# Kernel tuning notes

Hardware: AMD Instinct MI355X
Metric: run time of the kernel (lower is better)

Reference implementation:

```python
import jax, jax.numpy as jnp
import numpy as np

B, C_IN, L = 8, 64, 4096
C_OUT, HEADS = 64, 3
E = 524288
T_DIM = 256
N = B * L
EPS = 1e-5
NEG_SLOPE = 0.2  # PyG GATConv default negative_slope


def setup_inputs() -> dict:
    key = jax.random.key(0)
    ks = jax.random.split(key, 12)
    x = jax.random.normal(ks[0], (B, C_IN, L), jnp.float32)
    time_emb = jax.random.normal(ks[1], (B, T_DIM), jnp.float32)
    edge_index = jax.random.randint(ks[2], (2, E), 0, N, dtype=jnp.int32)
    # GATConv params: lin maps in -> heads*out; att_src/att_dst per head
    W_lin = jax.random.normal(ks[3], (C_IN, HEADS * C_OUT), jnp.float32) / np.sqrt(C_IN)
    att_src = jax.random.normal(ks[4], (1, HEADS, C_OUT), jnp.float32) / np.sqrt(C_OUT)
    att_dst = jax.random.normal(ks[5], (1, HEADS, C_OUT), jnp.float32) / np.sqrt(C_OUT)
    bias = jnp.zeros((C_OUT,), jnp.float32)
    # time projection (computed but unused in the source forward)
    tp_W = jax.random.normal(ks[6], (T_DIM, C_OUT), jnp.float32) / np.sqrt(T_DIM)
    tp_b = jnp.zeros((C_OUT,), jnp.float32)
    # BatchNorm1d affine params (training-mode batch stats)
    gamma = jnp.ones((C_OUT,), jnp.float32)
    beta = jnp.zeros((C_OUT,), jnp.float32)
    return {"x": x, "time_emb": time_emb, "edge_index": edge_index,
            "W_lin": W_lin, "att_src": att_src, "att_dst": att_dst,
            "bias": bias, "tp_W": tp_W, "tp_b": tp_b,
            "gamma": gamma, "beta": beta}


def reference(x, time_emb, edge_index, W_lin, att_src, att_dst, bias, tp_W, tp_b, gamma, beta):
    b, c, l = x.shape
    n = b * l
    # time projection: present in source but its result is never used
    _t = (time_emb @ tp_W + tp_b)[:, :, None]  # [b, C_OUT, 1] (dead)
    h = (x.reshape(-1, c) @ W_lin).reshape(n, HEADS, C_OUT)  # [N,H,C]
    a_src = (h * att_src).sum(-1)  # [N,H]
    a_dst = (h * att_dst).sum(-1)  # [N,H]
    # add self loops (PyG default add_self_loops=True)
    loops = jnp.arange(n, dtype=edge_index.dtype)
    src = jnp.concatenate([edge_index[0], loops])
    dst = jnp.concatenate([edge_index[1], loops])
    e = a_src[src] + a_dst[dst]                        # [E+N, H]
    e = jnp.where(e > 0, e, NEG_SLOPE * e)             # LeakyReLU
    emax = jax.ops.segment_max(e, dst, num_segments=n)  # every node has a self loop
    ex = jnp.exp(e - emax[dst])
    denom = jax.ops.segment_sum(ex, dst, num_segments=n)
    alpha = ex / denom[dst]                            # segment softmax over dst
    msg = alpha[:, :, None] * h[src]                   # [E+N, H, C]
    out = jax.ops.segment_sum(msg, dst, num_segments=n)  # [N,H,C]
    out = out.mean(axis=1) + bias                      # concat=False -> head mean
    # BatchNorm1d (training mode: biased batch stats)
    mu = out.mean(axis=0)
    var = ((out - mu) ** 2).mean(axis=0)
    out = (out - mu) / jnp.sqrt(var + EPS) * gamma + beta
    out = jax.nn.relu(out)
    return out.reshape(b, -1, l)
```

## Files before the change

kernel.cpp:

```cpp
#include <hip/hip_runtime.h>

#define N_NODES 32768
#define E_EDGES 524288
#define HC 192
#define NEG_SLOPE 0.2f
#define BN_EPS 1e-5f
#define PAD 64

typedef _Float16 f16;
typedef __attribute__((ext_vector_type(8))) _Float16 v8h;
typedef __attribute__((ext_vector_type(4))) float    v4f;

#define SCAT_BLOCKS 512
#define ASCORE_BLOCKS 512
#define FUSED_BLOCKS (SCAT_BLOCKS + ASCORE_BLOCKS)
#define NODE_BLOCKS 8192
#define GEMM_BLOCKS 512
#define APPLY_BLOCKS 512

__device__ __forceinline__ float lrelu(float v) { return v > 0.f ? v : NEG_SLOPE * v; }

__device__ __forceinline__ float wave_sum(float v) {
#pragma unroll
    for (int off = 32; off > 0; off >>= 1) v += __shfl_xor(v, off);
    return v;
}

__global__ __launch_bounds__(256, 4) void k_fused(
        const int* __restrict__ esrc, const int* __restrict__ edst,
        int* __restrict__ cnt, unsigned short* __restrict__ csr_pad,
        const float* __restrict__ x, const float* __restrict__ W,
        const float* __restrict__ att_s, const float* __restrict__ att_d,
        f16* __restrict__ x16, float* __restrict__ a_src, float* __restrict__ a_dst,
        f16* __restrict__ Wp, float* __restrict__ gp1, float* __restrict__ gp2) {
    const int bid = blockIdx.x;
    if (bid < SCAT_BLOCKS) {
        const int base = bid * 1024 + threadIdx.x;
        int s0 = esrc[base];       int d0 = edst[base];
        int s1 = esrc[base + 256]; int d1 = edst[base + 256];
        int s2 = esrc[base + 512]; int d2 = edst[base + 512];
        int s3 = esrc[base + 768]; int d3 = edst[base + 768];
        int p0 = atomicAdd(&cnt[d0], 1);
        int p1 = atomicAdd(&cnt[d1], 1);
        int p2 = atomicAdd(&cnt[d2], 1);
        int p3 = atomicAdd(&cnt[d3], 1);
        if (p0 < PAD) csr_pad[d0 * PAD + p0] = (unsigned short)s0;
        if (p1 < PAD) csr_pad[d1 * PAD + p1] = (unsigned short)s1;
        if (p2 < PAD) csr_pad[d2 * PAD + p2] = (unsigned short)s2;
        if (p3 < PAD) csr_pad[d3 * PAD + p3] = (unsigned short)s3;
        return;
    }
    const int gid = bid - SCAT_BLOCKS;
    __shared__ float us[3][64], ud[3][64];
    if (threadIdx.x < 192) {
        const int h = threadIdx.x >> 6, k = threadIdx.x & 63;
        const float* wr = W + k * HC + h * 64;
        const float* ap = att_s + h * 64;
        const float* dp = att_d + h * 64;
        float su = 0.f, du = 0.f;
#pragma unroll
        for (int ch = 0; ch < 64; ch++) {
            float w = wr[ch];
            su = fmaf(w, ap[ch], su);
            du = fmaf(w, dp[ch], du);
        }
        us[h][k] = su; ud[h][k] = du;
    }
    if (gid == 0) {
        float4 z4 = make_float4(0.f, 0.f, 0.f, 0.f);
#pragma unroll
        for (int i = 0; i < 4; i++) {
            ((float4*)gp1)[threadIdx.x * 4 + i] = z4;
            ((float4*)gp2)[threadIdx.x * 4 + i] = z4;
        }
        for (int idx = threadIdx.x; idx < 1536; idx += 256) {
            const int kfct = idx >> 6, ln = idx & 63;
            const int kf = kfct >> 2, ct = kfct & 3;
            const int qq = ln >> 4, nn = ln & 15;
#pragma unroll
            for (int j = 0; j < 8; j++) {
                int kp = kf * 32 + qq * 8 + j;
                int h = kp >> 6, kk = kp & 63;
                Wp[(size_t)idx * 8 + j] = (f16)W[kk * HC + h * 64 + ct * 16 + nn];
            }
        }
    }
    __syncthreads();
    const int lane = threadIdx.x & 63, wv = threadIdx.x >> 6;
    const float u0 = us[0][lane], u1 = us[1][lane], u2 = us[2][lane];
    const float d0 = ud[0][lane], d1 = ud[1][lane], d2 = ud[2][lane];
    const int nbase = (gid * 4 + wv) * 16;
#pragma unroll 1
    for (int t = 0; t < 16; t++) {
        const int n = nbase + t;
        const float xv = x[n * 64 + lane];
        x16[n * 64 + lane] = (f16)xv;
        float s0 = wave_sum(xv * u0), s1 = wave_sum(xv * u1), s2 = wave_sum(xv * u2);
        float t0 = wave_sum(xv * d0), t1 = wave_sum(xv * d1), t2 = wave_sum(xv * d2);
        if (lane == 0) {
            ((float4*)a_src)[n] = make_float4(s0, s1, s2, 0.f);
            ((float4*)a_dst)[n] = make_float4(t0, t1, t2, 0.f);
        }
    }
}

__global__ __launch_bounds__(256, 8) void k_node(
        const f16* __restrict__ x16,
        const float* __restrict__ a_src,
        const float* __restrict__ a_dst,
        const int* __restrict__ cnt,
        const unsigned short* __restrict__ csr_pad,
        f16* __restrict__ Z) {
    const int lane = threadIdx.x & 63;
    const int wv = threadIdx.x >> 6;
    const int n = blockIdx.x * 4 + wv;

    int deg = cnt[n]; if (deg > PAD) deg = PAD;
    const unsigned short* __restrict__ row = csr_pad + n * PAD;

    const float ad0 = a_dst[n * 4 + 0], ad1 = a_dst[n * 4 + 1], ad2 = a_dst[n * 4 + 2];

    float ws0 = __expf(lrelu(a_src[n * 4 + 0] + ad0));
    float ws1 = __expf(lrelu(a_src[n * 4 + 1] + ad1));
    float ws2 = __expf(lrelu(a_src[n * 4 + 2] + ad2));

    int s = 0;
    float w0 = 0.f, w1 = 0.f, w2 = 0.f;
    if (lane < deg) {
        s = (int)row[lane];
        float4 as = ((const float4*)a_src)[s];
        w0 = __expf(lrelu(as.x + ad0));
        w1 = __expf(lrelu(as.y + ad1));
        w2 = __expf(lrelu(as.z + ad2));
    }
    float den0 = ws0 + wave_sum(w0);
    float den1 = ws1 + wave_sum(w1);
    float den2 = ws2 + wave_sum(w2);
    const float i0 = 1.f / (3.f * den0);
    const float i1 = 1.f / (3.f * den1);
    const float i2 = 1.f / (3.f * den2);

    __shared__ float4 wsl[4][64];
    wsl[wv][lane] = make_float4(w0 * i0, w1 * i1, w2 * i2, __int_as_float(s));

    const float xs = (float)x16[n * 64 + lane];
    float z0 = ws0 * i0 * xs, z1 = ws1 * i1 * xs, z2 = ws2 * i2 * xs;

    int j = 0;
    for (; j + 8 <= deg; j += 8) {
        int sj[8]; float xv[8];
#pragma unroll
        for (int u = 0; u < 8; u++) sj[u] = __builtin_amdgcn_readlane(s, j + u);
#pragma unroll
        for (int u = 0; u < 8; u++) xv[u] = (float)x16[(size_t)sj[u] * 64 + lane];
#pragma unroll
        for (int u = 0; u < 8; u++) {
            float4 wj = wsl[wv][j + u];
            z0 = fmaf(wj.x, xv[u], z0);
            z1 = fmaf(wj.y, xv[u], z1);
            z2 = fmaf(wj.z, xv[u], z2);
        }
    }
    for (; j < deg; j++) {
        int sa = __builtin_amdgcn_readlane(s, j);
        float xa = (float)x16[(size_t)sa * 64 + lane];
        float4 wj = wsl[wv][j];
        z0 = fmaf(wj.x, xa, z0);
        z1 = fmaf(wj.y, xa, z1);
        z2 = fmaf(wj.z, xa, z2);
    }

    f16* zr = Z + (size_t)n * HC;
    zr[lane]       = (f16)z0;
    zr[64 + lane]  = (f16)z1;
    zr[128 + lane] = (f16)z2;
}

__global__ __launch_bounds__(256, 4) void k_gemm(
        const f16* __restrict__ Z, const f16* __restrict__ Wp,
        const float* __restrict__ bias,
        float* __restrict__ out_pre,
        float* __restrict__ gp1, float* __restrict__ gp2) {
    const int lane = threadIdx.x & 63, wv = threadIdx.x >> 6;
    const int q = lane >> 4, nl = lane & 15;
    const int n0 = (blockIdx.x * 4 + wv) * 16;

    v4f C[4] = {{0.f,0.f,0.f,0.f},{0.f,0.f,0.f,0.f},{0.f,0.f,0.f,0.f},{0.f,0.f,0.f,0.f}};
#pragma unroll
    for (int kf = 0; kf < 6; kf++) {
        v8h zb = *(const v8h*)(Z + (size_t)(n0 + nl) * HC + kf * 32 + q * 8);
#pragma unroll
        for (int ct = 0; ct < 4; ct++) {
            v8h wa = *(const v8h*)(Wp + ((size_t)(kf * 4 + ct) * 64 + lane) * 8);
            C[ct] = __builtin_amdgcn_mfma_f32_16x16x32_f16(wa, zb, C[ct], 0, 0, 0);
        }
    }

    __shared__ float bs[4][64], bq[4][64];
#pragma unroll
    for (int ct = 0; ct < 4; ct++) {
        const int ch0 = ct * 16 + q * 4;
        float4 bv = *(const float4*)(bias + ch0);
        float o0 = C[ct][0] + bv.x, o1 = C[ct][1] + bv.y;
        float o2 = C[ct][2] + bv.z, o3 = C[ct][3] + bv.w;
        *(float4*)(out_pre + (size_t)(n0 + nl) * 64 + ch0) = make_float4(o0, o1, o2, o3);
        float r0 = o0, r1 = o1, r2 = o2, r3 = o3;
        float s0 = o0 * o0, s1 = o1 * o1, s2 = o2 * o2, s3 = o3 * o3;
#pragma unroll
        for (int off = 1; off < 16; off <<= 1) {
            r0 += __shfl_xor(r0, off); r1 += __shfl_xor(r1, off);
            r2 += __shfl_xor(r2, off); r3 += __shfl_xor(r3, off);
            s0 += __shfl_xor(s0, off); s1 += __shfl_xor(s1, off);
            s2 += __shfl_xor(s2, off); s3 += __shfl_xor(s3, off);
        }
        if (nl == 0) {
            bs[wv][ch0 + 0] = r0; bs[wv][ch0 + 1] = r1;
            bs[wv][ch0 + 2] = r2; bs[wv][ch0 + 3] = r3;
            bq[wv][ch0 + 0] = s0; bq[wv][ch0 + 1] = s1;
            bq[wv][ch0 + 2] = s2; bq[wv][ch0 + 3] = s3;
        }
    }
    __syncthreads();
    if (threadIdx.x < 64) {
        int t = threadIdx.x;
        float s_ = bs[0][t] + bs[1][t] + bs[2][t] + bs[3][t];
        float q_ = bq[0][t] + bq[1][t] + bq[2][t] + bq[3][t];
        int slice = blockIdx.x & 63;
        atomicAdd(&gp1[slice * 64 + t], s_);
        atomicAdd(&gp2[slice * 64 + t], q_);
    }
}

__global__ __launch_bounds__(256) void k_apply(const float4* __restrict__ out_pre4,
                                               const float* __restrict__ gp1,
                                               const float* __restrict__ gp2,
                                               const float* __restrict__ gamma,
                                               const float* __restrict__ beta,
                                               float4* __restrict__ out4) {
    __shared__ float sc[64], sh[64];
    __shared__ float rs[256], rq[256];
    {
        const int t = threadIdx.x & 63, g = threadIdx.x >> 6;
        float s = 0.f, q = 0.f;
#pragma unroll
        for (int i = 0; i < 16; i++) {
            s += gp1[(g * 16 + i) * 64 + t];
            q += gp2[(g * 16 + i) * 64 + t];
        }
        rs[threadIdx.x] = s;
        rq[threadIdx.x] = q;
    }
    __syncthreads();
    if (threadIdx.x < 64) {
        int t = threadIdx.x;
        float s = rs[t] + rs[64 + t] + rs[128 + t] + rs[192 + t];
        float q = rq[t] + rq[64 + t] + rq[128 + t] + rq[192 + t];
        const float inv_n = 1.0f / (float)N_NODES;
        float mu = s * inv_n;
        float var = q * inv_n - mu * mu;
        float invstd = 1.0f / sqrtf(var + BN_EPS);
        float scale = invstd * gamma[t];
        sc[t] = scale;
        sh[t] = beta[t] - mu * scale;
    }
    __syncthreads();
    const int total = N_NODES * 64 / 4;
    for (int idx = blockIdx.x * 256 + threadIdx.x; idx < total; idx += APPLY_BLOCKS * 256) {
        int c0 = (idx * 4) & 63;
        float4 v = out_pre4[idx];
        float4 r;
        r.x = fmaxf(v.x * sc[c0 + 0] + sh[c0 + 0], 0.f);
        r.y = fmaxf(v.y * sc[c0 + 1] + sh[c0 + 1], 0.f);
        r.z = fmaxf(v.z * sc[c0 + 2] + sh[c0 + 2], 0.f);
        r.w = fmaxf(v.w * sc[c0 + 3] + sh[c0 + 3], 0.f);
        out4[idx] = r;
    }
}

extern "C" void kernel_launch(void* const* d_in, const int* in_sizes, int n_in,
                              void* d_out, int out_size, void* d_ws, size_t ws_size,
                              hipStream_t stream) {
    const float* x     = (const float*)d_in[0];
    const int*   ei    = (const int*)d_in[2];
    const float* W     = (const float*)d_in[3];
    const float* att_s = (const float*)d_in[4];
    const float* att_d = (const float*)d_in[5];
    const float* bias  = (const float*)d_in[6];
    const float* gamma = (const float*)d_in[9];
    const float* beta  = (const float*)d_in[10];
    float* out = (float*)d_out;

    char* ws = (char*)d_ws;
    size_t off = 0;
    auto alloc = [&](size_t bytes) -> void* {
        void* p = ws + off;
        off += (bytes + 255) & ~(size_t)255;
        return p;
    };
    f16*            x16     = (f16*)alloc((size_t)N_NODES * 64 * 2);
    float*          a_src   = (float*)alloc((size_t)N_NODES * 4 * 4);
    float*          a_dst   = (float*)alloc((size_t)N_NODES * 4 * 4);
    int*            cnt     = (int*)alloc((size_t)N_NODES * 4);
    unsigned short* csr_pad = (unsigned short*)alloc((size_t)N_NODES * PAD * 2);
    f16*            Z       = (f16*)alloc((size_t)N_NODES * HC * 2);
    f16*            Wp      = (f16*)alloc((size_t)1536 * 8 * 2);
    float*          out_pre = (float*)alloc((size_t)N_NODES * 64 * 4);
    float*          gp1     = (float*)alloc(64 * 64 * 4);
    float*          gp2     = (float*)alloc(64 * 64 * 4);

    hipMemsetAsync(cnt, 0, (size_t)N_NODES * 4, stream);

    k_fused<<<FUSED_BLOCKS, 256, 0, stream>>>(
        ei, ei + E_EDGES, cnt, csr_pad,
        x, W, att_s, att_d, x16, a_src, a_dst, Wp, gp1, gp2);
    k_node<<<NODE_BLOCKS, 256, 0, stream>>>(x16, a_src, a_dst, cnt, csr_pad, Z);
    k_gemm<<<GEMM_BLOCKS, 256, 0, stream>>>(Z, Wp, bias, out_pre, gp1, gp2);
    k_apply<<<APPLY_BLOCKS, 256, 0, stream>>>((const float4*)out_pre, gp1, gp2,
                                              gamma, beta, (float4*)out);
}
```

Before: 163.7 us.

## Fuse per-node attention aggregation with MFMA projection and pad edge counters

Attention aggregation and the W projection GEMM now run in one kernel. Each block aggregates 16 nodes into an LDS tile, then runs MFMA on it directly, so the global Z intermediate and one launch go away. Per-node edge counters are spaced 16 ints apart so scatter atomics hit separate cache lines, at the price of a larger memset. The scatter phase is regridded so some blocks handle two edges, and the GEMM epilogue does per-channel atomics straight into the slice partials.

```diff
diff --git a/kernel.cpp b/kernel.cpp
--- a/kernel.cpp
+++ b/kernel.cpp
@@ -11,12 +11,11 @@
 typedef __attribute__((ext_vector_type(8))) _Float16 v8h;
 typedef __attribute__((ext_vector_type(4))) float    v4f;
 
-#define SCAT_BLOCKS 512
-#define ASCORE_BLOCKS 512
-#define FUSED_BLOCKS (SCAT_BLOCKS + ASCORE_BLOCKS)
-#define NODE_BLOCKS 8192
-#define GEMM_BLOCKS 512
+#define SC_BLOCKS 1536
+#define K1_BLOCKS 2048
+#define K2_BLOCKS 2048
 #define APPLY_BLOCKS 512
+#define ZROW 200
 
 __device__ __forceinline__ float lrelu(float v) { return v > 0.f ? v : NEG_SLOPE * v; }
 
@@ -26,7 +25,7 @@
     return v;
 }
 
-__global__ __launch_bounds__(256, 4) void k_fused(
+__global__ __launch_bounds__(256, 8) void k_build(
         const int* __restrict__ esrc, const int* __restrict__ edst,
         int* __restrict__ cnt, unsigned short* __restrict__ csr_pad,
         const float* __restrict__ x, const float* __restrict__ W,
@@ -34,23 +33,19 @@
         f16* __restrict__ x16, float* __restrict__ a_src, float* __restrict__ a_dst,
         f16* __restrict__ Wp, float* __restrict__ gp1, float* __restrict__ gp2) {
     const int bid = blockIdx.x;
-    if (bid < SCAT_BLOCKS) {
-        const int base = bid * 1024 + threadIdx.x;
-        int s0 = esrc[base];       int d0 = edst[base];
-        int s1 = esrc[base + 256]; int d1 = edst[base + 256];
-        int s2 = esrc[base + 512]; int d2 = edst[base + 512];
-        int s3 = esrc[base + 768]; int d3 = edst[base + 768];
-        int p0 = atomicAdd(&cnt[d0], 1);
-        int p1 = atomicAdd(&cnt[d1], 1);
-        int p2 = atomicAdd(&cnt[d2], 1);
-        int p3 = atomicAdd(&cnt[d3], 1);
+    if (bid < SC_BLOCKS) {
+        int i = bid * 256 + threadIdx.x;
+        int s0 = esrc[i], d0 = edst[i];
+        int s1 = 0, d1 = 0;
+        const bool two = (bid < 512);
+        if (two) { s1 = esrc[i + 393216]; d1 = edst[i + 393216]; }
+        int p0 = atomicAdd(&cnt[d0 << 4], 1);
+        int p1 = two ? atomicAdd(&cnt[d1 << 4], 1) : 0;
         if (p0 < PAD) csr_pad[d0 * PAD + p0] = (unsigned short)s0;
-        if (p1 < PAD) csr_pad[d1 * PAD + p1] = (unsigned short)s1;
-        if (p2 < PAD) csr_pad[d2 * PAD + p2] = (unsigned short)s2;
-        if (p3 < PAD) csr_pad[d3 * PAD + p3] = (unsigned short)s3;
+        if (two && p1 < PAD) csr_pad[d1 * PAD + p1] = (unsigned short)s1;
         return;
     }
-    const int gid = bid - SCAT_BLOCKS;
+    const int gid = bid - SC_BLOCKS;
     __shared__ float us[3][64], ud[3][64];
     if (threadIdx.x < 192) {
         const int h = threadIdx.x >> 6, k = threadIdx.x & 63;
@@ -104,130 +99,110 @@
     }
 }
 
-__global__ __launch_bounds__(256, 8) void k_node(
+__global__ __launch_bounds__(256, 8) void k_agg(
         const f16* __restrict__ x16,
         const float* __restrict__ a_src,
         const float* __restrict__ a_dst,
         const int* __restrict__ cnt,
         const unsigned short* __restrict__ csr_pad,
-        f16* __restrict__ Z) {
-    const int lane = threadIdx.x & 63;
-    const int wv = threadIdx.x >> 6;
-    const int n = blockIdx.x * 4 + wv;
-
-    int deg = cnt[n]; if (deg > PAD) deg = PAD;
-    const unsigned short* __restrict__ row = csr_pad + n * PAD;
-
-    const float ad0 = a_dst[n * 4 + 0], ad1 = a_dst[n * 4 + 1], ad2 = a_dst[n * 4 + 2];
-
-    float ws0 = __expf(lrelu(a_src[n * 4 + 0] + ad0));
-    float ws1 = __expf(lrelu(a_src[n * 4 + 1] + ad1));
-    float ws2 = __expf(lrelu(a_src[n * 4 + 2] + ad2));
-
-    int s = 0;
-    float w0 = 0.f, w1 = 0.f, w2 = 0.f;
-    if (lane < deg) {
-        s = (int)row[lane];
-        float4 as = ((const float4*)a_src)[s];
-        w0 = __expf(lrelu(as.x + ad0));
-        w1 = __expf(lrelu(as.y + ad1));
-        w2 = __expf(lrelu(as.z + ad2));
-    }
-    float den0 = ws0 + wave_sum(w0);
-    float den1 = ws1 + wave_sum(w1);
-    float den2 = ws2 + wave_sum(w2);
-    const float i0 = 1.f / (3.f * den0);
-    const float i1 = 1.f / (3.f * den1);
-    const float i2 = 1.f / (3.f * den2);
-
-    __shared__ float4 wsl[4][64];
-    wsl[wv][lane] = make_float4(w0 * i0, w1 * i1, w2 * i2, __int_as_float(s));
-
-    const float xs = (float)x16[n * 64 + lane];
-    float z0 = ws0 * i0 * xs, z1 = ws1 * i1 * xs, z2 = ws2 * i2 * xs;
-
-    int j = 0;
-    for (; j + 8 <= deg; j += 8) {
-        int sj[8]; float xv[8];
-#pragma unroll
-        for (int u = 0; u < 8; u++) sj[u] = __builtin_amdgcn_readlane(s, j + u);
-#pragma unroll
-        for (int u = 0; u < 8; u++) xv[u] = (float)x16[(size_t)sj[u] * 64 + lane];
-#pragma unroll
-        for (int u = 0; u < 8; u++) {
-            float4 wj = wsl[wv][j + u];
-            z0 = fmaf(wj.x, xv[u], z0);
-            z1 = fmaf(wj.y, xv[u], z1);
-            z2 = fmaf(wj.z, xv[u], z2);
-        }
-    }
-    for (; j < deg; j++) {
-        int sa = __builtin_amdgcn_readlane(s, j);
-        float xa = (float)x16[(size_t)sa * 64 + lane];
-        float4 wj = wsl[wv][j];
-        z0 = fmaf(wj.x, xa, z0);
-        z1 = fmaf(wj.y, xa, z1);
-        z2 = fmaf(wj.z, xa, z2);
-    }
-
-    f16* zr = Z + (size_t)n * HC;
-    zr[lane]       = (f16)z0;
-    zr[64 + lane]  = (f16)z1;
-    zr[128 + lane] = (f16)z2;
-}
-
-__global__ __launch_bounds__(256, 4) void k_gemm(
-        const f16* __restrict__ Z, const f16* __restrict__ Wp,
+        const f16* __restrict__ Wp,
         const float* __restrict__ bias,
         float* __restrict__ out_pre,
         float* __restrict__ gp1, float* __restrict__ gp2) {
-    const int lane = threadIdx.x & 63, wv = threadIdx.x >> 6;
+    const int lane = threadIdx.x & 63;
+    const int wv = threadIdx.x >> 6;
+    const int bid = blockIdx.x;
+    const int n0 = bid * 16;
+
+    __shared__ f16 zlds[16][ZROW];
+    __shared__ float4 wsl[4][64];
+
+#pragma unroll 1
+    for (int r = 0; r < 4; r++) {
+        const int n = n0 + (r << 2) + wv;
+        int deg = cnt[n << 4]; if (deg > PAD) deg = PAD;
+        const unsigned short* __restrict__ row = csr_pad + n * PAD;
+        const float ad0 = a_dst[n * 4 + 0], ad1 = a_dst[n * 4 + 1], ad2 = a_dst[n * 4 + 2];
+        float ws0 = __expf(lrelu(a_src[n * 4 + 0] + ad0));
+        float ws1 = __expf(lrelu(a_src[n * 4 + 1] + ad1));
+        float ws2 = __expf(lrelu(a_src[n * 4 + 2] + ad2));
+        int s = 0;
+        float w0 = 0.f, w1 = 0.f, w2 = 0.f;
+        if (lane < deg) {
+            s = (int)row[lane];
+            float4 as = ((const float4*)a_src)[s];
+            w0 = __expf(lrelu(as.x + ad0));
+            w1 = __expf(lrelu(as.y + ad1));
+            w2 = __expf(lrelu(as.z + ad2));
+        }
+        float den0 = ws0 + wave_sum(w0);
+        float den1 = ws1 + wave_sum(w1);
+        float den2 = ws2 + wave_sum(w2);
+        const float i0 = 1.f / (3.f * den0);
+        const float i1 = 1.f / (3.f * den1);
+        const float i2 = 1.f / (3.f * den2);
+        wsl[wv][lane] = make_float4(w0 * i0, w1 * i1, w2 * i2, 0.f);
+        const float xs = (float)x16[(size_t)n * 64 + lane];
+        float z0 = ws0 * i0 * xs, z1 = ws1 * i1 * xs, z2 = ws2 * i2 * xs;
+        int j = 0;
+        for (; j + 8 <= deg; j += 8) {
+            int sj[8]; float xv[8];
+#pragma unroll
+            for (int u = 0; u < 8; u++) sj[u] = __builtin_amdgcn_readlane(s, j + u);
+#pragma unroll
+            for (int u = 0; u < 8; u++) xv[u] = (float)x16[(size_t)sj[u] * 64 + lane];
+#pragma unroll
+            for (int u = 0; u < 8; u++) {
+                float4 wj = wsl[wv][j + u];
+                z0 = fmaf(wj.x, xv[u], z0);
+                z1 = fmaf(wj.y, xv[u], z1);
+                z2 = fmaf(wj.z, xv[u], z2);
+            }
+        }
+        for (; j < deg; j++) {
+            int sa = __builtin_amdgcn_readlane(s, j);
+            float xa = (float)x16[(size_t)sa * 64 + lane];
+            float4 wj = wsl[wv][j];
+            z0 = fmaf(wj.x, xa, z0);
+            z1 = fmaf(wj.y, xa, z1);
+            z2 = fmaf(wj.z, xa, z2);
+        }
+        const int rl = (r << 2) + wv;
+        zlds[rl][lane]       = (f16)z0;
+        zlds[rl][64 + lane]  = (f16)z1;
+        zlds[rl][128 + lane] = (f16)z2;
+    }
+    __syncthreads();
+
     const int q = lane >> 4, nl = lane & 15;
-    const int n0 = (blockIdx.x * 4 + wv) * 16;
-
-    v4f C[4] = {{0.f,0.f,0.f,0.f},{0.f,0.f,0.f,0.f},{0.f,0.f,0.f,0.f},{0.f,0.f,0.f,0.f}};
+    v4f C = {0.f, 0.f, 0.f, 0.f};
 #pragma unroll
     for (int kf = 0; kf < 6; kf++) {
-        v8h zb = *(const v8h*)(Z + (size_t)(n0 + nl) * HC + kf * 32 + q * 8);
-#pragma unroll
-        for (int ct = 0; ct < 4; ct++) {
-            v8h wa = *(const v8h*)(Wp + ((size_t)(kf * 4 + ct) * 64 + lane) * 8);
-            C[ct] = __builtin_amdgcn_mfma_f32_16x16x32_f16(wa, zb, C[ct], 0, 0, 0);
-        }
-    }
-
-    __shared__ float bs[4][64], bq[4][64];
-#pragma unroll
-    for (int ct = 0; ct < 4; ct++) {
-        const int ch0 = ct * 16 + q * 4;
-        float4 bv = *(const float4*)(bias + ch0);
-        float o0 = C[ct][0] + bv.x, o1 = C[ct][1] + bv.y;
-        float o2 = C[ct][2] + bv.z, o3 = C[ct][3] + bv.w;
-        *(float4*)(out_pre + (size_t)(n0 + nl) * 64 + ch0) = make_float4(o0, o1, o2, o3);
-        float r0 = o0, r1 = o1, r2 = o2, r3 = o3;
-        float s0 = o0 * o0, s1 = o1 * o1, s2 = o2 * o2, s3 = o3 * o3;
-#pragma unroll
-        for (int off = 1; off < 16; off <<= 1) {
-            r0 += __shfl_xor(r0, off); r1 += __shfl_xor(r1, off);
-            r2 += __shfl_xor(r2, off); r3 += __shfl_xor(r3, off);
-            s0 += __shfl_xor(s0, off); s1 += __shfl_xor(s1, off);
-            s2 += __shfl_xor(s2, off); s3 += __shfl_xor(s3, off);
-        }
-        if (nl == 0) {
-            bs[wv][ch0 + 0] = r0; bs[wv][ch0 + 1] = r1;
-            bs[wv][ch0 + 2] = r2; bs[wv][ch0 + 3] = r3;
-            bq[wv][ch0 + 0] = s0; bq[wv][ch0 + 1] = s1;
-            bq[wv][ch0 + 2] = s2; bq[wv][ch0 + 3] = s3;
-        }
-    }
-    __syncthreads();
-    if (threadIdx.x < 64) {
-        int t = threadIdx.x;
-        float s_ = bs[0][t] + bs[1][t] + bs[2][t] + bs[3][t];
-        float q_ = bq[0][t] + bq[1][t] + bq[2][t] + bq[3][t];
-        int slice = blockIdx.x & 63;
-        atomicAdd(&gp1[slice * 64 + t], s_);
-        atomicAdd(&gp2[slice * 64 + t], q_);
+        v8h zb = *(const v8h*)(&zlds[nl][kf * 32 + q * 8]);
+        v8h wa = *(const v8h*)(Wp + ((size_t)(kf * 4 + wv) * 64 + lane) * 8);
+        C = __builtin_amdgcn_mfma_f32_16x16x32_f16(wa, zb, C, 0, 0, 0);
+    }
+    const int ch0 = wv * 16 + q * 4;
+    float4 bv = *(const float4*)(bias + ch0);
+    float o0 = C[0] + bv.x, o1 = C[1] + bv.y, o2 = C[2] + bv.z, o3 = C[3] + bv.w;
+    *(float4*)(out_pre + (size_t)(n0 + nl) * 64 + ch0) = make_float4(o0, o1, o2, o3);
+    float r0 = o0, r1 = o1, r2 = o2, r3 = o3;
+    float q0 = o0 * o0, q1 = o1 * o1, q2 = o2 * o2, q3 = o3 * o3;
+#pragma unroll
+    for (int off = 1; off < 16; off <<= 1) {
+        r0 += __shfl_xor(r0, off); r1 += __shfl_xor(r1, off);
+        r2 += __shfl_xor(r2, off); r3 += __shfl_xor(r3, off);
+        q0 += __shfl_xor(q0, off); q1 += __shfl_xor(q1, off);
+        q2 += __shfl_xor(q2, off); q3 += __shfl_xor(q3, off);
+    }
+    if (nl == 0) {
+        const int slice = bid & 63;
+        float* g1 = gp1 + slice * 64 + ch0;
+        float* g2 = gp2 + slice * 64 + ch0;
+        atomicAdd(&g1[0], r0); atomicAdd(&g1[1], r1);
+        atomicAdd(&g1[2], r2); atomicAdd(&g1[3], r3);
+        atomicAdd(&g2[0], q0); atomicAdd(&g2[1], q1);
+        atomicAdd(&g2[2], q2); atomicAdd(&g2[3], q3);
     }
 }
 
@@ -297,24 +272,23 @@
         off += (bytes + 255) & ~(size_t)255;
         return p;
     };
+    int*            cnt     = (int*)alloc((size_t)N_NODES * 16 * 4);
+    unsigned short* csr_pad = (unsigned short*)alloc((size_t)N_NODES * PAD * 2);
     f16*            x16     = (f16*)alloc((size_t)N_NODES * 64 * 2);
     float*          a_src   = (float*)alloc((size_t)N_NODES * 4 * 4);
     float*          a_dst   = (float*)alloc((size_t)N_NODES * 4 * 4);
-    int*            cnt     = (int*)alloc((size_t)N_NODES * 4);
-    unsigned short* csr_pad = (unsigned short*)alloc((size_t)N_NODES * PAD * 2);
-    f16*            Z       = (f16*)alloc((size_t)N_NODES * HC * 2);
     f16*            Wp      = (f16*)alloc((size_t)1536 * 8 * 2);
-    float*          out_pre = (float*)alloc((size_t)N_NODES * 64 * 4);
     float*          gp1     = (float*)alloc(64 * 64 * 4);
     float*          gp2     = (float*)alloc(64 * 64 * 4);
-
-    hipMemsetAsync(cnt, 0, (size_t)N_NODES * 4, stream);
-
-    k_fused<<<FUSED_BLOCKS, 256, 0, stream>>>(
+    float*          out_pre = (float*)alloc((size_t)N_NODES * 64 * 4);
+
+    hipMemsetAsync(cnt, 0, (size_t)N_NODES * 16 * 4, stream);
+
+    k_build<<<K1_BLOCKS, 256, 0, stream>>>(
         ei, ei + E_EDGES, cnt, csr_pad,
         x, W, att_s, att_d, x16, a_src, a_dst, Wp, gp1, gp2);
-    k_node<<<NODE_BLOCKS, 256, 0, stream>>>(x16, a_src, a_dst, cnt, csr_pad, Z);
-    k_gemm<<<GEMM_BLOCKS, 256, 0, stream>>>(Z, Wp, bias, out_pre, gp1, gp2);
+    k_agg<<<K2_BLOCKS, 256, 0, stream>>>(x16, a_src, a_dst, cnt, csr_pad, Wp,
+                                         bias, out_pre, gp1, gp2);
     k_apply<<<APPLY_BLOCKS, 256, 0, stream>>>((const float4*)out_pre, gp1, gp2,
                                               gamma, beta, (float4*)out);
 }
```

New measurement: 161.6 us. Within noise of the previous version (-1.3%).
